# Kernel tuning notes

Measured on AMD Instinct MI355X. Metric: run time of the kernel, lower is better.

Reference implementation:

```python
import jax, jax.numpy as jnp
import numpy as np

EMB_DIM, TREE_DIM, OUT_DIM, VOCAB = 256, 256, 3, 10000
T, B, LEVELS = 255, 128, 8  # complete binary tree of depth 8, 128 trees per input


def _build_forest():
    # node j = T-1-heap(j): root (heap 0) is the LAST node so stack_last_h picks the root.
    heap = np.arange(T)
    depth = np.floor(np.log2(heap + 1)).astype(np.int64)  # 0..7
    node_order = np.empty(T, dtype=np.int64)
    node_order[T - 1 - heap] = (LEVELS - 1) - depth       # leaves=0, root=7
    internal = np.arange((T - 1) // 2)                     # heaps with two children
    parent = np.repeat(T - 1 - internal, 2)
    child = np.stack([T - 1 - (2 * internal + 1), T - 1 - (2 * internal + 2)], 1).reshape(-1)
    edges = np.stack([parent, child], axis=1)              # (254, 2)
    edge_order = node_order[parent]
    offs = (np.arange(B) * T)[:, None, None]
    adj = (edges[None] + offs).reshape(-1, 2)              # (B*254, 2)
    return np.tile(node_order, B), adj, np.tile(edge_order, B)


def setup_inputs() -> dict:
    key = jax.random.key(0)
    ks = jax.random.split(key, 16)
    no, adj, eo = _build_forest()
    D = TREE_DIM
    s_e = 1.0 / np.sqrt(EMB_DIM)
    s_t = 1.0 / np.sqrt(D)
    return {
        'feat_cube': jax.random.randint(ks[0], (B * T,), 0, VOCAB),
        'feat_a': jax.random.randint(ks[1], (B * T,), 0, VOCAB),
        'feat_b': jax.random.randint(ks[2], (B * T,), 0, VOCAB),
        'node_order': jnp.asarray(no),
        'adjacency_list': jnp.asarray(adj),
        'edge_order': jnp.asarray(eo),
        'num_levels': LEVELS,
        'num_trees': B,
        'emb': jax.random.normal(ks[3], (VOCAB, EMB_DIM), jnp.float32),
        'W_iou': jax.random.normal(ks[4], (3 * D, EMB_DIM), jnp.float32) * s_e,
        'b_iou': jnp.zeros((3 * D,), jnp.float32),
        'U_iou': jax.random.normal(ks[5], (3 * D, D), jnp.float32) * s_t,
        'W_f': jax.random.normal(ks[6], (D, EMB_DIM), jnp.float32) * s_e,
        'b_f': jnp.zeros((D,), jnp.float32),
        'U_f': jax.random.normal(ks[7], (D, D), jnp.float32) * s_t,
        'fc1_w': jax.random.normal(ks[8], (D // 2, D), jnp.float32) * s_t,
        'fc1_b': jnp.zeros((D // 2,), jnp.float32),
        'fc2_w': jax.random.normal(ks[9], (OUT_DIM, D // 2), jnp.float32) * (1.0 / np.sqrt(D // 2)),
        'fc2_b': jnp.zeros((OUT_DIM,), jnp.float32),
    }


def _tree_lstm(x, node_order, parents, children, edge_order, W_iou, b_iou, U_iou, W_f, b_f, U_f, num_levels):
    # Child-sum TreeLSTM, evaluated level by level (leaves first). Dense masked
    # formulation: per level we update only nodes with node_order==lvl; edge
    # contributions are masked before segment_sum (same math as the torch loop).
    N = x.shape[0]
    D = U_f.shape[0]
    x_iou = x @ W_iou.T + b_iou            # (N, 3D), precomputed once
    x_f = x @ W_f.T + b_f                  # (N, D)
    h = jnp.zeros((N, D), x.dtype)
    c = jnp.zeros((N, D), x.dtype)
    for lvl in range(num_levels):
        emask = (edge_order == lvl)[:, None].astype(x.dtype)
        ch = h[children]                   # (E, D) gather of child hidden
        cc = c[children]
        f = jax.nn.sigmoid(x_f[parents] + ch @ U_f.T)
        h_sum = jax.ops.segment_sum(ch * emask, parents, num_segments=N)
        c_sum = jax.ops.segment_sum(f * cc * emask, parents, num_segments=N)
        i, o, u = jnp.split(x_iou + h_sum @ U_iou.T, 3, axis=1)
        c_new = jax.nn.sigmoid(i) * jnp.tanh(u) + c_sum
        h_new = jax.nn.sigmoid(o) * jnp.tanh(c_new)
        nmask = (node_order == lvl)[:, None]
        h = jnp.where(nmask, h_new, h)
        c = jnp.where(nmask, c_new, c)
    return h, c


def reference(feat_cube, feat_a, feat_b, node_order, adjacency_list, edge_order,
              num_levels, num_trees, emb, W_iou, b_iou, U_iou, W_f, b_f, U_f,
              fc1_w, fc1_b, fc2_w, fc2_b):
    parents = adjacency_list[:, 0]
    children = adjacency_list[:, 1]

    def run_tree(feat):
        h, _ = _tree_lstm(emb[feat], node_order, parents, children, edge_order,
                          W_iou, b_iou, U_iou, W_f, b_f, U_f, num_levels)
        # stack_last_h: last node of each tree (= root with our labeling)
        return h.reshape(num_trees, -1, h.shape[-1])[:, -1, :]

    h_c = run_tree(feat_cube)
    h_a = run_tree(feat_a)
    h_b = run_tree(feat_b)
    # h_c (1,D) @ (h_a (D,1) @ h_b (1,D)) == (h_c . h_a) * h_b, fused einsum
    h = jnp.einsum('bi,bi,bj->bj', h_c, h_a, h_b)
    hid = jax.nn.relu(h @ fc1_w.T + fc1_b)
    logits = jax.nn.relu(hid @ fc2_w.T + fc2_b)
    return logits  # (num_trees, out_dim)
```

## Files before the change

kernel.cpp:

```cpp
#include <hip/hip_runtime.h>
#include <hip/hip_bf16.h>

typedef __hip_bfloat16 bf16;
typedef unsigned short u16;
typedef __attribute__((ext_vector_type(8))) short s8;
typedef __attribute__((ext_vector_type(4))) float f4;

#define NRUNS 3
#define NTREE 128
#define TT    255
#define DD    256
#define VPAD  10016
#define PAD   258

__device__ __forceinline__ float bits2f(u16 b){ union{unsigned u; float f;} x; x.u = ((unsigned)b)<<16; return x.f; }
__device__ __forceinline__ u16   f2bits(float f){ bf16 h = __float2bfloat16(f); return *(u16*)&h; }
__device__ __forceinline__ float sigm(float x){ return 1.f/(1.f+__expf(-x)); }
__device__ __forceinline__ float tanh_(float x){ return 1.f - 2.f/(__expf(2.f*x)+1.f); }

__global__ void k_detect(const u16* __restrict__ raw, int* __restrict__ flag){
    int t = threadIdx.x;
    int hit = 0;
    if (t < 128){
        u16 w = raw[2*t];
        int e = (w >> 7) & 0xFF;
        hit = (e >= 100 && e <= 141) ? 1 : 0;
    }
    __shared__ int cnt;
    if (t == 0) cnt = 0;
    __syncthreads();
    atomicAdd(&cnt, hit);
    __syncthreads();
    if (t == 0) flag[0] = (cnt >= 64) ? 1 : 0;
}

__device__ __forceinline__ u16 cvt1b(const void* p, int i, int isb){
    return isb ? ((const u16*)p)[i] : f2bits(((const float*)p)[i]);
}
__device__ __forceinline__ float cvt1f(const void* p, int i, int isb){
    return isb ? bits2f(((const u16*)p)[i]) : ((const float*)p)[i];
}

#define L_EMB  (10000*256)
#define L_EMBP (VPAD*256)
#define L_WIOU (768*256)
#define L_UIOU (768*256)
#define L_WF   (256*256)
#define L_UF   (256*256)
#define L_ALL  (L_EMBP + L_WIOU + L_UIOU + L_WF + L_UF)
__global__ void k_cvtb(const void* __restrict__ s0, const void* __restrict__ s1,
                       const void* __restrict__ s2, const void* __restrict__ s3,
                       const void* __restrict__ s4,
                       u16* __restrict__ d0, u16* __restrict__ d1, u16* __restrict__ d2,
                       u16* __restrict__ d3, u16* __restrict__ d4,
                       const int* __restrict__ flag){
    int isb = flag[0];
    for (int i = blockIdx.x*blockDim.x + threadIdx.x; i < L_ALL; i += gridDim.x*blockDim.x){
        int j = i;
        if (j < L_EMBP){ d0[j] = (j < L_EMB) ? cvt1b(s0, j, isb) : (u16)0; continue; } j -= L_EMBP;
        if (j < L_WIOU){ d1[j] = cvt1b(s1, j, isb); continue; } j -= L_WIOU;
        if (j < L_UIOU){ d2[j] = cvt1b(s2, j, isb); continue; } j -= L_UIOU;
        if (j < L_WF){ d3[j] = cvt1b(s3, j, isb); continue; } j -= L_WF;
        d4[j] = cvt1b(s4, j, isb);
    }
}

#define S_BIOU 768
#define S_BF   256
#define S_F1W  (128*256)
#define S_F1B  128
#define S_F2W  (3*128)
#define S_F2B  3
#define S_ALL  (S_BIOU+S_BF+S_F1W+S_F1B+S_F2W+S_F2B)
__global__ void k_small(const void* __restrict__ s0, const void* __restrict__ s1,
                        const void* __restrict__ s2, const void* __restrict__ s3,
                        const void* __restrict__ s4, const void* __restrict__ s5,
                        float* __restrict__ d0, float* __restrict__ d1, float* __restrict__ d2,
                        float* __restrict__ d3, float* __restrict__ d4, float* __restrict__ d5,
                        const int* __restrict__ flag){
    int isb = flag[0];
    for (int i = blockIdx.x*blockDim.x + threadIdx.x; i < S_ALL; i += gridDim.x*blockDim.x){
        int j = i;
        if (j < S_BIOU){ d0[j] = cvt1f(s0, j, isb); continue; } j -= S_BIOU;
        if (j < S_BF){ d1[j] = cvt1f(s1, j, isb); continue; } j -= S_BF;
        if (j < S_F1W){ d2[j] = cvt1f(s2, j, isb); continue; } j -= S_F1W;
        if (j < S_F1B){ d3[j] = cvt1f(s3, j, isb); continue; } j -= S_F1B;
        if (j < S_F2W){ d4[j] = cvt1f(s4, j, isb); continue; } j -= S_F2W;
        d5[j] = cvt1f(s5, j, isb);
    }
}

__device__ __forceinline__ s8 ldB16(const u16* p){
    union { uint4 q; s8 v; } u;
    u.q = *(const uint4*)p;
    return u.v;
}
__device__ __forceinline__ s8 ldsA(const u16* p){
    union { unsigned w[4]; s8 v; } u;
    u.w[0] = *(const unsigned*)(p);
    u.w[1] = *(const unsigned*)(p+2);
    u.w[2] = *(const unsigned*)(p+4);
    u.w[3] = *(const unsigned*)(p+6);
    return u.v;
}
#define MFMA(acc,a,b) acc = __builtin_amdgcn_mfma_f32_16x16x32_bf16(a, b, acc, 0, 0, 0)

__global__ __launch_bounds__(512, 4)
void k_vocab(const u16* __restrict__ embb,
             const u16* __restrict__ Wiou, const u16* __restrict__ Wfm,
             u16* __restrict__ E_iou, u16* __restrict__ E_f)
{
    const int t = threadIdx.x, w = t>>6, lane = t&63, ln = lane&15, q = lane>>4;
    const int r0 = blockIdx.x*32, n0 = w*128;

    const u16* Bp[8];
    #pragma unroll
    for (int nt = 0; nt < 8; nt++){
        int n = n0 + nt*16 + ln;
        Bp[nt] = (n < 768) ? (Wiou + (size_t)n*DD) : (Wfm + (size_t)(n-768)*DD);
    }
    const u16* a0p = embb + (size_t)(r0+ln)*DD;
    const u16* a1p = embb + (size_t)(r0+16+ln)*DD;

    f4 acc[8][2];
    #pragma unroll
    for (int nt = 0; nt < 8; nt++){ acc[nt][0] = (f4){0,0,0,0}; acc[nt][1] = (f4){0,0,0,0}; }

    #pragma unroll 2
    for (int ks = 0; ks < 8; ks++){
        int ko = ks*32 + q*8;
        s8 a0 = ldB16(a0p + ko);
        s8 a1 = ldB16(a1p + ko);
        #pragma unroll
        for (int nt = 0; nt < 8; nt++){
            s8 bb = ldB16(Bp[nt] + ko);
            MFMA(acc[nt][0], a0, bb);
            MFMA(acc[nt][1], a1, bb);
        }
    }
    #pragma unroll
    for (int nt = 0; nt < 8; nt++){
        int n = n0 + nt*16 + ln;
        #pragma unroll
        for (int ms = 0; ms < 2; ms++)
          #pragma unroll
          for (int r = 0; r < 4; r++){
            int v = r0 + ms*16 + q*4 + r;
            u16 val = f2bits(acc[nt][ms][r]);
            if (n < 768) E_iou[(size_t)v*768 + n] = val;
            else         E_f[(size_t)v*DD + (n-768)] = val;
        }
    }
}

__global__ __launch_bounds__(512, 4)
void k_lvl(int lvl, int cLog,
           const int* __restrict__ f0, const int* __restrict__ f1, const int* __restrict__ f2,
           const u16* __restrict__ E_iou, const u16* __restrict__ E_f,
           const u16* __restrict__ Uiou, const u16* __restrict__ Ufm,
           const float* __restrict__ biou_f, const float* __restrict__ bf_f,
           const u16* __restrict__ hsum_in, const u16* __restrict__ fcsum_in,
           u16* __restrict__ hsum_out, u16* __restrict__ fcsum_out,
           u16* __restrict__ hroot)
{
    __shared__ u16 hs[32*PAD];
    const int t = threadIdx.x, w = t>>6, lane = t&63, ln = lane&15, q = lane>>4;
    const int cnt = 1 << cLog, S = 256 - 2*cnt;
    const int r0 = blockIdx.x*32, d0 = w*32;
    const bool haveU = (lvl > 0);
    const bool haveP = (lvl < 7);

    int feat[2][4], featp[2][2];
    #pragma unroll
    for (int ms = 0; ms < 2; ms++)
      #pragma unroll
      for (int r = 0; r < 4; r++){
        int rho = r0 + ms*16 + q*4 + r;
        int run = rho >> (7+cLog);
        int rem = rho & ((1<<(7+cLog)) - 1);
        int b = rem >> cLog, jj = rem & (cnt-1);
        const int* fp = (run==0) ? f0 : ((run==1) ? f1 : f2);
        feat[ms][r] = fp[b*TT + S + jj];
        if (haveP && (r&1)==0)
            featp[ms][r>>1] = fp[b*TT + (256-cnt) + (jj>>1)];
      }

    f4 acc[6][2];
    #pragma unroll
    for (int nt = 0; nt < 6; nt++){ acc[nt][0] = (f4){0,0,0,0}; acc[nt][1] = (f4){0,0,0,0}; }
    if (haveU){
        const u16* a0p = hsum_in + (size_t)(r0+ln)*DD;
        const u16* a1p = hsum_in + (size_t)(r0+16+ln)*DD;
        const u16* Bp[6];
        #pragma unroll
        for (int nt = 0; nt < 6; nt++){
            int n = (nt>>1)*256 + d0 + (nt&1)*16 + ln;
            Bp[nt] = Uiou + (size_t)n*DD;
        }
        #pragma unroll 2
        for (int ks = 0; ks < 8; ks++){
            int ko = ks*32 + q*8;
            s8 a0 = ldB16(a0p + ko);
            s8 a1 = ldB16(a1p + ko);
            #pragma unroll
            for (int nt = 0; nt < 6; nt++){
                s8 bb = ldB16(Bp[nt] + ko);
                MFMA(acc[nt][0], a0, bb);
                MFMA(acc[nt][1], a1, bb);
            }
        }
    }

    float cv[2][2][4];
    #pragma unroll
    for (int nc = 0; nc < 2; nc++){
        int d = d0 + nc*16 + ln;
        float bi = biou_f[d], bo = biou_f[256+d], bu = biou_f[512+d];
        #pragma unroll
        for (int ms = 0; ms < 2; ms++){
            float hv[4];
            #pragma unroll
            for (int r = 0; r < 4; r++){
                int rho = r0 + ms*16 + q*4 + r;
                size_t eb = (size_t)feat[ms][r]*768 + d;
                float iv = acc[0+nc][ms][r] + bits2f(E_iou[eb])       + bi;
                float ov = acc[2+nc][ms][r] + bits2f(E_iou[eb + 256]) + bo;
                float uv = acc[4+nc][ms][r] + bits2f(E_iou[eb + 512]) + bu;
                float cs = haveU ? bits2f(fcsum_in[(size_t)rho*DD + d]) : 0.f;
                float c = sigm(iv)*tanh_(uv) + cs;
                float h = sigm(ov)*tanh_(c);
                cv[nc][ms][r] = c;
                hv[r] = h;
                if (haveP) hs[(ms*16 + q*4 + r)*PAD + d] = f2bits(h);
                else       hroot[(size_t)rho*DD + d] = f2bits(h);
            }
            if (haveP){
                int prow = (r0>>1) + ms*8 + q*2;
                hsum_out[(size_t)prow*DD + d]     = f2bits(hv[0] + hv[1]);
                hsum_out[(size_t)(prow+1)*DD + d] = f2bits(hv[2] + hv[3]);
            }
        }
    }

    if (haveP){
        __syncthreads();
        f4 hacc[2][2];
        #pragma unroll
        for (int nt = 0; nt < 2; nt++){ hacc[nt][0] = (f4){0,0,0,0}; hacc[nt][1] = (f4){0,0,0,0}; }
        const u16* Bf0 = Ufm + (size_t)(d0 + ln)*DD;
        const u16* Bf1 = Ufm + (size_t)(d0 + 16 + ln)*DD;
        #pragma unroll 2
        for (int ks = 0; ks < 8; ks++){
            int ko = ks*32 + q*8;
            s8 a0 = ldsA(&hs[ln*PAD + ko]);
            s8 a1 = ldsA(&hs[(16+ln)*PAD + ko]);
            s8 b0 = ldB16(Bf0 + ko);
            s8 b1 = ldB16(Bf1 + ko);
            MFMA(hacc[0][0], a0, b0); MFMA(hacc[0][1], a1, b0);
            MFMA(hacc[1][0], a0, b1); MFMA(hacc[1][1], a1, b1);
        }
        #pragma unroll
        for (int nc = 0; nc < 2; nc++){
            int d = d0 + nc*16 + ln;
            float bfv = bf_f[d];
            #pragma unroll
            for (int ms = 0; ms < 2; ms++){
                float fs0, fs1;
                #pragma unroll
                for (int r = 0; r < 4; r++){
                    float ef = bits2f(E_f[(size_t)featp[ms][r>>1]*DD + d]);
                    float fc = sigm(ef + bfv + hacc[nc][ms][r]) * cv[nc][ms][r];
                    if (r == 0) fs0 = fc;
                    else if (r == 1) fs0 += fc;
                    else if (r == 2) fs1 = fc;
                    else fs1 += fc;
                }
                int prow = (r0>>1) + ms*8 + q*2;
                fcsum_out[(size_t)prow*DD + d]     = f2bits(fs0);
                fcsum_out[(size_t)(prow+1)*DD + d] = f2bits(fs1);
            }
        }
    }
}

__global__ __launch_bounds__(256)
void k_final(const u16* __restrict__ hroot,
             const float* __restrict__ fc1w, const float* __restrict__ fc1b,
             const float* __restrict__ fc2w, const float* __restrict__ fc2b,
             void* __restrict__ out, const int* __restrict__ flag)
{
    int b = blockIdx.x, t = threadIdx.x;
    __shared__ float sprod[DD];
    __shared__ float shb[DD];
    __shared__ float shid[128];
    float hc  = bits2f(hroot[(0*NTREE + b)*DD + t]);
    float ha  = bits2f(hroot[(1*NTREE + b)*DD + t]);
    float hbv = bits2f(hroot[(2*NTREE + b)*DD + t]);
    sprod[t] = hc * ha;
    shb[t]   = hbv;
    __syncthreads();
    for (int s = 128; s > 0; s >>= 1){
        if (t < s) sprod[t] += sprod[t + s];
        __syncthreads();
    }
    float dot = sprod[0];
    if (t < 128){
        float acc = fc1b[t];
        for (int k = 0; k < DD; k++)
            acc = fmaf(dot * shb[k], fc1w[t*DD + k], acc);
        shid[t] = fmaxf(acc, 0.f);
    }
    __syncthreads();
    if (t < 3){
        float acc = fc2b[t];
        for (int j = 0; j < 128; j++)
            acc = fmaf(fc2w[t*128 + j], shid[j], acc);
        float v = fmaxf(acc, 0.f);
        if (flag[0]) ((bf16*)out)[b*3 + t] = __float2bfloat16(v);
        else         ((float*)out)[b*3 + t] = v;
    }
}

extern "C" void kernel_launch(void* const* d_in, const int* in_sizes, int n_in,
                              void* d_out, int out_size, void* d_ws, size_t ws_size,
                              hipStream_t stream)
{
    const int* f0 = (const int*)d_in[0];
    const int* f1 = (const int*)d_in[1];
    const int* f2 = (const int*)d_in[2];
    const void* emb  = d_in[8];
    const void* Wiou = d_in[9];
    const void* biou = d_in[10];
    const void* Uiou = d_in[11];
    const void* Wf   = d_in[12];
    const void* bfv  = d_in[13];
    const void* Uf   = d_in[14];
    const void* fc1w = d_in[15];
    const void* fc1b = d_in[16];
    const void* fc2w = d_in[17];
    const void* fc2b = d_in[18];

    char* base = (char*)d_ws;
    size_t off = 0;
    auto take = [&](size_t bytes) -> char* {
        char* p = base + off;
        off = (off + bytes + 255) & ~(size_t)255;
        return p;
    };
    int*   flag   = (int*)  take(256);
    u16*   embb   = (u16*)  take((size_t)L_EMBP*2);
    u16*   wioub  = (u16*)  take((size_t)L_WIOU*2);
    u16*   uioub  = (u16*)  take((size_t)L_UIOU*2);
    u16*   wfb    = (u16*)  take((size_t)L_WF*2);
    u16*   ufb    = (u16*)  take((size_t)L_UF*2);
    float* biou_f = (float*)take(S_BIOU*4);
    float* bf_f   = (float*)take(S_BF*4);
    float* fc1w_f = (float*)take(S_F1W*4);
    float* fc1b_f = (float*)take(S_F1B*4);
    float* fc2w_f = (float*)take(S_F2W*4);
    float* fc2b_f = (float*)take(S_F2B*4);
    u16*   E_iou  = (u16*)  take((size_t)VPAD*768*2);
    u16*   E_f    = (u16*)  take((size_t)VPAD*256*2);
    u16*   HA     = (u16*)  take((size_t)24576*DD*2);
    u16*   HB     = (u16*)  take((size_t)12288*DD*2);
    u16*   FA     = (u16*)  take((size_t)24576*DD*2);
    u16*   FB     = (u16*)  take((size_t)12288*DD*2);
    u16*   hroot  = (u16*)  take((size_t)NRUNS*NTREE*DD*2);

    k_detect<<<1, 256, 0, stream>>>((const u16*)emb, flag);
    k_cvtb<<<2048, 256, 0, stream>>>(emb, Wiou, Uiou, Wf, Uf,
                                     embb, wioub, uioub, wfb, ufb, flag);
    k_small<<<135, 256, 0, stream>>>(biou, bfv, fc1w, fc1b, fc2w, fc2b,
                                     biou_f, bf_f, fc1w_f, fc1b_f, fc2w_f, fc2b_f, flag);
    k_vocab<<<VPAD/32, 512, 0, stream>>>(embb, wioub, wfb, E_iou, E_f);

    for (int lvl = 0; lvl <= 7; lvl++){
        int cLog = 7 - lvl;
        int rows = NRUNS*NTREE*(128 >> lvl);
        int blocks = rows / 32;
        int pe = lvl & 1;
        u16* hs_o = pe ? HB : HA;
        u16* fc_o = pe ? FB : FA;
        const u16* hs_i = pe ? HA : HB;
        const u16* fc_i = pe ? FA : FB;
        k_lvl<<<blocks, 512, 0, stream>>>(lvl, cLog, f0, f1, f2,
                                          E_iou, E_f, uioub, ufb,
                                          biou_f, bf_f,
                                          hs_i, fc_i, hs_o, fc_o, hroot);
    }
    k_final<<<NTREE, 256, 0, stream>>>(hroot, fc1w_f, fc1b_f, fc2w_f, fc2b_f, d_out, flag);
}
```

Baseline: 489.2 us.

## Precompute leaf-level LSTM state per vocabulary entry and replace level-0 kernel

Leaf nodes depend only on their token, so their h, c and U_f·h are now computed once per vocabulary row inside the vocab GEMM kernel, staged through shared memory. A new elementwise edge kernel then gathers these per-token tables to form the level-1 child sums, replacing the level-0 tree kernel. The vocab kernel's output stores also become vectorised 16-byte writes through LDS. The cost is a larger vocab kernel with lower occupancy (launch bounds 2) and three extra vocabulary-sized buffers.

```diff
diff --git a/kernel.cpp b/kernel.cpp
--- a/kernel.cpp
+++ b/kernel.cpp
@@ -12,6 +12,7 @@
 #define DD    256
 #define VPAD  10016
 #define PAD   258
+#define ESTR  1026
 
 __device__ __forceinline__ float bits2f(u16 b){ union{unsigned u; float f;} x; x.u = ((unsigned)b)<<16; return x.f; }
 __device__ __forceinline__ u16   f2bits(float f){ bf16 h = __float2bfloat16(f); return *(u16*)&h; }
@@ -105,11 +106,15 @@
 }
 #define MFMA(acc,a,b) acc = __builtin_amdgcn_mfma_f32_16x16x32_bf16(a, b, acc, 0, 0, 0)
 
-__global__ __launch_bounds__(512, 4)
-void k_vocab(const u16* __restrict__ embb,
-             const u16* __restrict__ Wiou, const u16* __restrict__ Wfm,
-             u16* __restrict__ E_iou, u16* __restrict__ E_f)
+__global__ __launch_bounds__(512, 2)
+void k_vocab2(const u16* __restrict__ embb,
+              const u16* __restrict__ Wiou, const u16* __restrict__ Wfm,
+              const u16* __restrict__ Ufm,  const float* __restrict__ biou_f,
+              u16* __restrict__ E_iou, u16* __restrict__ E_f,
+              u16* __restrict__ H0, u16* __restrict__ C0, u16* __restrict__ HU0)
 {
+    __shared__ u16 es[32*ESTR];
+    __shared__ u16 hs[32*PAD];
     const int t = threadIdx.x, w = t>>6, lane = t&63, ln = lane&15, q = lane>>4;
     const int r0 = blockIdx.x*32, n0 = w*128;
 
@@ -121,11 +126,9 @@
     }
     const u16* a0p = embb + (size_t)(r0+ln)*DD;
     const u16* a1p = embb + (size_t)(r0+16+ln)*DD;
-
     f4 acc[8][2];
     #pragma unroll
     for (int nt = 0; nt < 8; nt++){ acc[nt][0] = (f4){0,0,0,0}; acc[nt][1] = (f4){0,0,0,0}; }
-
     #pragma unroll 2
     for (int ks = 0; ks < 8; ks++){
         int ko = ks*32 + q*8;
@@ -144,13 +147,112 @@
         #pragma unroll
         for (int ms = 0; ms < 2; ms++)
           #pragma unroll
+          for (int r = 0; r < 4; r++)
+            es[(ms*16 + q*4 + r)*ESTR + n] = f2bits(acc[nt][ms][r]);
+    }
+    __syncthreads();
+
+    for (int it = 0; it < 8; it++){
+        int idx = it*512 + t;
+        int row = idx >> 7, c = idx & 127;
+        int n = c*8;
+        union { unsigned w4[4]; uint4 q4; } u;
+        const u16* p = &es[row*ESTR + n];
+        u.w4[0] = *(const unsigned*)(p);
+        u.w4[1] = *(const unsigned*)(p+2);
+        u.w4[2] = *(const unsigned*)(p+4);
+        u.w4[3] = *(const unsigned*)(p+6);
+        int vrow = r0 + row;
+        if (n < 768) *(uint4*)(E_iou + (size_t)vrow*768 + n) = u.q4;
+        else         *(uint4*)(E_f   + (size_t)vrow*DD + (n-768)) = u.q4;
+    }
+    for (int it = 0; it < 2; it++){
+        int idx = it*512 + t;
+        int row = idx >> 5, c = idx & 31;
+        int d = c*8;
+        u16 hv[8], cv[8];
+        #pragma unroll
+        for (int j = 0; j < 8; j++){
+            float iv = bits2f(es[row*ESTR + d + j])       + biou_f[d+j];
+            float ov = bits2f(es[row*ESTR + 256 + d + j]) + biou_f[256+d+j];
+            float uv = bits2f(es[row*ESTR + 512 + d + j]) + biou_f[512+d+j];
+            float cc = sigm(iv)*tanh_(uv);
+            float hh = sigm(ov)*tanh_(cc);
+            cv[j] = f2bits(cc);
+            hv[j] = f2bits(hh);
+            hs[row*PAD + d + j] = hv[j];
+        }
+        union { u16 a[8]; uint4 q4; } uc, uh;
+        #pragma unroll
+        for (int j = 0; j < 8; j++){ uc.a[j] = cv[j]; uh.a[j] = hv[j]; }
+        *(uint4*)(C0 + (size_t)(r0+row)*DD + d) = uc.q4;
+        *(uint4*)(H0 + (size_t)(r0+row)*DD + d) = uh.q4;
+    }
+    __syncthreads();
+
+    const int d0 = w*32;
+    f4 hacc[2][2];
+    #pragma unroll
+    for (int nt = 0; nt < 2; nt++){ hacc[nt][0] = (f4){0,0,0,0}; hacc[nt][1] = (f4){0,0,0,0}; }
+    const u16* Bf0 = Ufm + (size_t)(d0 + ln)*DD;
+    const u16* Bf1 = Ufm + (size_t)(d0 + 16 + ln)*DD;
+    #pragma unroll 2
+    for (int ks = 0; ks < 8; ks++){
+        int ko = ks*32 + q*8;
+        s8 a0 = ldsA(&hs[ln*PAD + ko]);
+        s8 a1 = ldsA(&hs[(16+ln)*PAD + ko]);
+        s8 b0 = ldB16(Bf0 + ko);
+        s8 b1 = ldB16(Bf1 + ko);
+        MFMA(hacc[0][0], a0, b0); MFMA(hacc[0][1], a1, b0);
+        MFMA(hacc[1][0], a0, b1); MFMA(hacc[1][1], a1, b1);
+    }
+    #pragma unroll
+    for (int nc = 0; nc < 2; nc++){
+        int d = d0 + nc*16 + ln;
+        #pragma unroll
+        for (int ms = 0; ms < 2; ms++)
+          #pragma unroll
           for (int r = 0; r < 4; r++){
-            int v = r0 + ms*16 + q*4 + r;
-            u16 val = f2bits(acc[nt][ms][r]);
-            if (n < 768) E_iou[(size_t)v*768 + n] = val;
-            else         E_f[(size_t)v*DD + (n-768)] = val;
-        }
-    }
+            int vrow = r0 + ms*16 + q*4 + r;
+            HU0[(size_t)vrow*DD + d] = f2bits(hacc[nc][ms][r]);
+        }
+    }
+}
+
+__global__ __launch_bounds__(512, 4)
+void k_edge0(const int* __restrict__ f0, const int* __restrict__ f1, const int* __restrict__ f2,
+             const u16* __restrict__ E_f, const u16* __restrict__ H0,
+             const u16* __restrict__ C0,  const u16* __restrict__ HU0,
+             const float* __restrict__ bf_f,
+             u16* __restrict__ hsum_out, u16* __restrict__ fcsum_out)
+{
+    int gid = blockIdx.x*512 + threadIdx.x;
+    int row = gid >> 5, ch = gid & 31, d = ch*8;
+    int run = row >> 13, rem = row & 8191, b = rem >> 6, jj = rem & 63;
+    const int* fp = (run==0) ? f0 : ((run==1) ? f1 : f2);
+    int fo = fp[b*TT + 128 + jj];
+    int v1 = fp[b*TT + 2*jj];
+    int v2 = fp[b*TT + 2*jj + 1];
+    s8 ef  = ldB16(E_f + (size_t)fo*DD + d);
+    s8 hu1 = ldB16(HU0 + (size_t)v1*DD + d);
+    s8 hu2 = ldB16(HU0 + (size_t)v2*DD + d);
+    s8 c1  = ldB16(C0  + (size_t)v1*DD + d);
+    s8 c2  = ldB16(C0  + (size_t)v2*DD + d);
+    s8 h1  = ldB16(H0  + (size_t)v1*DD + d);
+    s8 h2  = ldB16(H0  + (size_t)v2*DD + d);
+    union { u16 a[8]; uint4 q4; } uh, uf;
+    #pragma unroll
+    for (int j = 0; j < 8; j++){
+        float e  = bits2f((u16)ef[j]) + bf_f[d+j];
+        float fa = sigm(e + bits2f((u16)hu1[j]));
+        float fb = sigm(e + bits2f((u16)hu2[j]));
+        float fc = fa*bits2f((u16)c1[j]) + fb*bits2f((u16)c2[j]);
+        float hsv = bits2f((u16)h1[j]) + bits2f((u16)h2[j]);
+        uf.a[j] = f2bits(fc);
+        uh.a[j] = f2bits(hsv);
+    }
+    *(uint4*)(hsum_out  + (size_t)row*DD + d) = uh.q4;
+    *(uint4*)(fcsum_out + (size_t)row*DD + d) = uf.q4;
 }
 
 __global__ __launch_bounds__(512, 4)
@@ -360,7 +462,10 @@
     float* fc2w_f = (float*)take(S_F2W*4);
     float* fc2b_f = (float*)take(S_F2B*4);
     u16*   E_iou  = (u16*)  take((size_t)VPAD*768*2);
-    u16*   E_f    = (u16*)  take((size_t)VPAD*256*2);
+    u16*   E_f    = (u16*)  take((size_t)VPAD*DD*2);
+    u16*   H0     = (u16*)  take((size_t)VPAD*DD*2);
+    u16*   C0     = (u16*)  take((size_t)VPAD*DD*2);
+    u16*   HU0    = (u16*)  take((size_t)VPAD*DD*2);
     u16*   HA     = (u16*)  take((size_t)24576*DD*2);
     u16*   HB     = (u16*)  take((size_t)12288*DD*2);
     u16*   FA     = (u16*)  take((size_t)24576*DD*2);
@@ -372,9 +477,11 @@
                                      embb, wioub, uioub, wfb, ufb, flag);
     k_small<<<135, 256, 0, stream>>>(biou, bfv, fc1w, fc1b, fc2w, fc2b,
                                      biou_f, bf_f, fc1w_f, fc1b_f, fc2w_f, fc2b_f, flag);
-    k_vocab<<<VPAD/32, 512, 0, stream>>>(embb, wioub, wfb, E_iou, E_f);
-
-    for (int lvl = 0; lvl <= 7; lvl++){
+    k_vocab2<<<VPAD/32, 512, 0, stream>>>(embb, wioub, wfb, ufb, biou_f,
+                                          E_iou, E_f, H0, C0, HU0);
+    k_edge0<<<24576*32/512, 512, 0, stream>>>(f0, f1, f2, E_f, H0, C0, HU0, bf_f, HA, FA);
+
+    for (int lvl = 1; lvl <= 7; lvl++){
         int cLog = 7 - lvl;
         int rows = NRUNS*NTREE*(128 >> lvl);
         int blocks = rows / 32;
```

Result: faster. 465.3 us (-4.9%).
